# Performance work log

Measured on AMD Instinct MI355X. Metric: run time of the kernel, lower is better.

## Reference

```python
import jax, jax.numpy as jnp
import numpy as np

N_NODES = 60000
N_EDGES = 240000
N_REL = 4
N_GRAPHS = 128
D_IN = 768
D_H = 256
N_LAYERS = 6


def setup_inputs() -> dict:
    key = jax.random.key(0)
    ks = jax.random.split(key, 16)
    x = jax.random.normal(ks[0], (N_NODES, D_IN), dtype=jnp.float32)
    edge_index = jax.random.randint(ks[1], (2, N_EDGES), 0, N_NODES, dtype=jnp.int64)
    edge_attr = jax.random.randint(ks[2], (N_EDGES,), 0, N_REL, dtype=jnp.int64)
    batch = jnp.sort(jax.random.randint(ks[3], (N_NODES,), 0, N_GRAPHS, dtype=jnp.int64))
    s0 = 1.0 / np.sqrt(D_IN)
    s1 = 1.0 / np.sqrt(D_H)
    w0 = jax.random.normal(ks[4], (N_REL, D_IN, D_H), dtype=jnp.float32) * s0
    root0 = jax.random.normal(ks[5], (D_IN, D_H), dtype=jnp.float32) * s0
    b0 = jnp.zeros((D_H,), jnp.float32)
    w_rest = jax.random.normal(ks[6], (N_LAYERS - 1, N_REL, D_H, D_H), dtype=jnp.float32) * s1
    root_rest = jax.random.normal(ks[7], (N_LAYERS - 1, D_H, D_H), dtype=jnp.float32) * s1
    b_rest = jnp.zeros((N_LAYERS - 1, D_H), jnp.float32)
    fc1_w = jax.random.normal(ks[8], (2 * D_H, 128), dtype=jnp.float32) * (1.0 / np.sqrt(2 * D_H))
    fc1_b = jnp.zeros((128,), jnp.float32)
    fc2_w = jax.random.normal(ks[9], (128, 1), dtype=jnp.float32) * (1.0 / np.sqrt(128))
    fc2_b = jnp.zeros((1,), jnp.float32)
    return {"x": x, "edge_index": edge_index, "edge_attr": edge_attr, "batch": batch,
            "w0": w0, "root0": root0, "b0": b0,
            "w_rest": w_rest, "root_rest": root_rest, "b_rest": b_rest,
            "fc1_w": fc1_w, "fc1_b": fc1_b, "fc2_w": fc2_w, "fc2_b": fc2_b}


def _rgcn(h, src, dst, rel, W, root, b):
    # PyG RGCNConv with aggr='mean': per-relation mean over incoming edges,
    # transformed by per-relation weight, plus root transform and bias.
    n = h.shape[0]
    seg = rel * n + dst                                   # combined (relation, target) segment id
    msgs = h[src]                                         # [E, d_in] gather
    agg = jax.ops.segment_sum(msgs, seg, num_segments=N_REL * n)
    agg = agg.reshape(N_REL, n, -1)                       # [R, N, d_in]
    cnt = jax.ops.segment_sum(jnp.ones_like(rel, jnp.float32), seg, num_segments=N_REL * n)
    cnt = cnt.reshape(N_REL, n, 1)
    mean = agg / jnp.maximum(cnt, 1.0)                    # mean aggregation; 0 for isolated nodes
    return jnp.einsum('rnd,rdo->no', mean, W) + h @ root + b


def reference(x, edge_index, edge_attr, batch, w0, root0, b0,
              w_rest, root_rest, b_rest, fc1_w, fc1_b, fc2_w, fc2_b):
    src, dst = edge_index[0], edge_index[1]
    h = jax.nn.relu(_rgcn(x, src, dst, edge_attr, w0, root0, b0))
    for i in range(N_LAYERS - 1):
        h = jax.nn.relu(_rgcn(h, src, dst, edge_attr, w_rest[i], root_rest[i], b_rest[i]))
    # global mean / max pooling over graphs
    sums = jax.ops.segment_sum(h, batch, num_segments=N_GRAPHS)
    cnt = jax.ops.segment_sum(jnp.ones((h.shape[0],), jnp.float32), batch, num_segments=N_GRAPHS)[:, None]
    h_mean = sums / jnp.maximum(cnt, 1.0)
    h_max = jax.ops.segment_max(h, batch, num_segments=N_GRAPHS)
    h_max = jnp.where(cnt > 0, h_max, 0.0)
    g = jnp.concatenate([h_mean, h_max], axis=1)          # [G, 512]
    out = jax.nn.relu(g @ fc1_w + fc1_b)                  # dropout is identity at inference
    out = out @ fc2_w + fc2_b
    return jax.nn.sigmoid(out.squeeze(-1))                # [G]
```

## Files before the change

kernel.cpp:

```cpp
#include <hip/hip_runtime.h>
#include <hip/hip_bf16.h>

#define N_NODES  60000
#define N_EDGES  240000
#define N_REL    4
#define N_GRAPHS 128
#define D_IN     768
#define D_H      256
#define N_LAYERS 6
#define M_PAD    60032
#define N_TOT    1280
#define BM_L     64
#define LDM      264

static inline int cdiv(int a, int b) { return (a + b - 1) / b; }

typedef __attribute__((ext_vector_type(8))) short short8;
typedef __attribute__((ext_vector_type(4))) float f32x4;

__device__ __forceinline__ float bf2f(unsigned short u) {
    union { unsigned int i; float f; } c; c.i = ((unsigned int)u) << 16; return c.f;
}
__device__ __forceinline__ float bflo(unsigned int u) {
    union { unsigned int i; float f; } c; c.i = u << 16; return c.f;
}
__device__ __forceinline__ float bfhi(unsigned int u) {
    union { unsigned int i; float f; } c; c.i = u & 0xffff0000u; return c.f;
}
__device__ __forceinline__ unsigned short f2bf(float f) {
    union { float f; unsigned int i; } c; c.f = f;
    unsigned int i = c.i;
    unsigned int r = (i + 0x7FFFu + ((i >> 16) & 1u)) >> 16;
    return (unsigned short)r;
}

__device__ __forceinline__ void gload16(const void* g, void* l) {
    __builtin_amdgcn_global_load_lds((const __attribute__((address_space(1))) void*)g,
                                     (__attribute__((address_space(3))) void*)l, 16, 0, 0);
}

__device__ __forceinline__ void accum32(float4* am, uint4 v0, uint4 v1, uint4 v2, uint4 v3) {
    am[0].x += bflo(v0.x); am[0].y += bfhi(v0.x);
    am[0].z += bflo(v0.y); am[0].w += bfhi(v0.y);
    am[1].x += bflo(v0.z); am[1].y += bfhi(v0.z);
    am[1].z += bflo(v0.w); am[1].w += bfhi(v0.w);
    am[2].x += bflo(v1.x); am[2].y += bfhi(v1.x);
    am[2].z += bflo(v1.y); am[2].w += bfhi(v1.y);
    am[3].x += bflo(v1.z); am[3].y += bfhi(v1.z);
    am[3].z += bflo(v1.w); am[3].w += bfhi(v1.w);
    am[4].x += bflo(v2.x); am[4].y += bfhi(v2.x);
    am[4].z += bflo(v2.y); am[4].w += bfhi(v2.y);
    am[5].x += bflo(v2.z); am[5].y += bfhi(v2.z);
    am[5].z += bflo(v2.w); am[5].w += bfhi(v2.w);
    am[6].x += bflo(v3.x); am[6].y += bfhi(v3.x);
    am[6].z += bflo(v3.y); am[6].w += bfhi(v3.y);
    am[7].x += bflo(v3.z); am[7].y += bfhi(v3.z);
    am[7].z += bflo(v3.w); am[7].w += bfhi(v3.w);
}

__global__ __launch_bounds__(512) void gemm_l0(
    const unsigned short* __restrict__ A,
    const unsigned short* __restrict__ Bt,
    const float* __restrict__ bias,
    unsigned short* __restrict__ out_root,
    unsigned short* __restrict__ out_msg,
    int K)
{
    __shared__ unsigned short As[128 * 32];
    __shared__ unsigned short Bs[256 * 32];

    const int tid  = threadIdx.x;
    const int wave = tid >> 6, lane = tid & 63;

    int b = blockIdx.x;
    int bm, bn;
    if (b < 2320) { int grp = b / 40, rem = b % 40; bm = (grp * 8 + (rem & 7)) * 128; bn = (rem >> 3) * 256; }
    else          { int rem = b - 2320; bm = (464 + rem % 5) * 128; bn = (rem / 5) * 256; }

    const int wm = (wave & 1) * 64, wn = (wave >> 1) * 64;

    const int lr = lane >> 2;
    const int kg = ((lane & 3) ^ ((lr ^ (lr >> 2)) & 3)) * 8;
    const unsigned short* gsrc[3];
    unsigned short* ldst[3];
    #pragma unroll
    for (int j = 0; j < 3; ++j) {
        int g = wave * 3 + j;
        if (g < 8) {
            gsrc[j] = A + (size_t)(bm + g * 16 + lr) * K + kg;
            ldst[j] = As + g * 16 * 32;
        } else {
            gsrc[j] = Bt + (size_t)(bn + (g - 8) * 16 + lr) * K + kg;
            ldst[j] = Bs + (g - 8) * 16 * 32;
        }
    }

    f32x4 acc[4][4] = {};
    const int fr = lane & 15;
    const int qsw = (((lane >> 4) ^ fr ^ (fr >> 2)) & 3) * 8;

    for (int k0 = 0; k0 < K; k0 += 32) {
        gload16(gsrc[0] + k0, ldst[0]);
        gload16(gsrc[1] + k0, ldst[1]);
        gload16(gsrc[2] + k0, ldst[2]);
        __syncthreads();

        short8 a[4], bb[4];
        #pragma unroll
        for (int t = 0; t < 4; ++t) {
            a[t]  = *(const short8*)&As[(wm + t * 16 + fr) * 32 + qsw];
            bb[t] = *(const short8*)&Bs[(wn + t * 16 + fr) * 32 + qsw];
        }
        #pragma unroll
        for (int mt = 0; mt < 4; ++mt)
            #pragma unroll
            for (int nt = 0; nt < 4; ++nt)
                acc[mt][nt] = __builtin_amdgcn_mfma_f32_16x16x32_bf16(
                    a[mt], bb[nt], acc[mt][nt], 0, 0, 0);
        __syncthreads();
    }

    const bool is_root = (bn == 0);
    #pragma unroll
    for (int mt = 0; mt < 4; ++mt) {
        #pragma unroll
        for (int nt = 0; nt < 4; ++nt) {
            int col = bn + wn + nt * 16 + fr;
            float bv = bias[col];
            #pragma unroll
            for (int r = 0; r < 4; ++r) {
                int row = bm + wm + mt * 16 + ((lane >> 4) << 2) + r;
                float v = acc[mt][nt][r] + bv;
                if (is_root) out_root[(size_t)row * 256 + col] = f2bf(v);
                else         out_msg[(size_t)row * 1024 + (col - 256)] = f2bf(v);
            }
        }
    }
}

__global__ __launch_bounds__(512) void rgcn_layer(
    const unsigned short* __restrict__ h,
    const unsigned short* __restrict__ Wl,
    const float* __restrict__ bias,
    const int* __restrict__ rp4,
    const int* __restrict__ e_srcs,
    const float* __restrict__ inv4,
    unsigned short* __restrict__ h_out)
{
    __shared__ unsigned short mt[BM_L * LDM];

    const int tid  = threadIdx.x;
    const int wave = tid >> 6, lane = tid & 63;
    const int bm = blockIdx.x * BM_L;

    const int node  = bm + lane;
    const int cq    = wave * 32;
    const bool valid = node < N_NODES;

    const int fr   = lane & 15;
    const int q8   = (lane >> 4) * 8;
    const int wcol = wave * 32;

    const unsigned short* w0p = Wl + (size_t)(wcol + fr) * N_TOT + q8;
    const unsigned short* w1p = Wl + (size_t)(wcol + 16 + fr) * N_TOT + q8;

    float4 iv = valid ? *(const float4*)&inv4[(size_t)node * 4]
                      : make_float4(1.f, 1.f, 1.f, 1.f);

    f32x4 acc[4][2] = {};

    for (int r = 0; r < 5; ++r) {
        float4 am[8];
        #pragma unroll
        for (int j = 0; j < 8; ++j) am[j] = make_float4(0.f, 0.f, 0.f, 0.f);

        if (r < 4) {
            if (valid) {
                int lo = rp4[(size_t)node * 4 + r];
                int hi = rp4[(size_t)node * 4 + r + 1];
                int e = lo;
                for (; e + 1 < hi; e += 2) {
                    const uint4* p0 = (const uint4*)(h + (size_t)e_srcs[e] * 256 + cq);
                    const uint4* p1 = (const uint4*)(h + (size_t)e_srcs[e + 1] * 256 + cq);
                    uint4 v0 = p0[0], v1 = p0[1], v2 = p0[2], v3 = p0[3];
                    uint4 u0 = p1[0], u1 = p1[1], u2 = p1[2], u3 = p1[3];
                    accum32(am, v0, v1, v2, v3);
                    accum32(am, u0, u1, u2, u3);
                }
                if (e < hi) {
                    const uint4* p0 = (const uint4*)(h + (size_t)e_srcs[e] * 256 + cq);
                    accum32(am, p0[0], p0[1], p0[2], p0[3]);
                }
            }
        } else {
            const uint4* p0 = (const uint4*)(h + (size_t)node * 256 + cq);
            accum32(am, p0[0], p0[1], p0[2], p0[3]);
        }
        float sc = (r == 0) ? iv.x : (r == 1) ? iv.y : (r == 2) ? iv.z
                 : (r == 3) ? iv.w : 1.f;

        __syncthreads();
        {
            unsigned short* dst = &mt[lane * LDM + cq];
            #pragma unroll
            for (int j = 0; j < 8; ++j) {
                ushort4 o;
                o.x = f2bf(am[j].x * sc); o.y = f2bf(am[j].y * sc);
                o.z = f2bf(am[j].z * sc); o.w = f2bf(am[j].w * sc);
                *(ushort4*)(dst + j * 4) = o;
            }
        }
        __syncthreads();

        const int rOff = (r << 8);
        #pragma unroll
        for (int kk = 0; kk < 8; ++kk) {
            short8 b0 = *(const short8*)(w0p + rOff + kk * 32);
            short8 b1 = *(const short8*)(w1p + rOff + kk * 32);
            short8 a[4];
            #pragma unroll
            for (int i = 0; i < 4; ++i)
                a[i] = *(const short8*)&mt[(i * 16 + fr) * LDM + kk * 32 + q8];
            #pragma unroll
            for (int i = 0; i < 4; ++i) {
                acc[i][0] = __builtin_amdgcn_mfma_f32_16x16x32_bf16(a[i], b0, acc[i][0], 0, 0, 0);
                acc[i][1] = __builtin_amdgcn_mfma_f32_16x16x32_bf16(a[i], b1, acc[i][1], 0, 0, 0);
            }
        }
    }

    #pragma unroll
    for (int i = 0; i < 4; ++i) {
        #pragma unroll
        for (int nt = 0; nt < 2; ++nt) {
            int col = wcol + nt * 16 + fr;
            float bv = bias[col];
            #pragma unroll
            for (int rg = 0; rg < 4; ++rg) {
                int row = bm + i * 16 + ((lane >> 4) << 2) + rg;
                float v = fmaxf(acc[i][nt][rg] + bv, 0.f);
                h_out[(size_t)row * 256 + col] = f2bf(v);
            }
        }
    }
}

__global__ void convert_x(const float* __restrict__ x, unsigned short* __restrict__ xb) {
    size_t i = ((size_t)blockIdx.x * 256 + threadIdx.x) * 4;
    if (i >= (size_t)M_PAD * D_IN) return;
    ushort4 o;
    if (i < (size_t)N_NODES * D_IN) {
        float4 v = *(const float4*)&x[i];
        o.x = f2bf(v.x); o.y = f2bf(v.y); o.z = f2bf(v.z); o.w = f2bf(v.w);
    } else {
        o.x = o.y = o.z = o.w = 0;
    }
    *(ushort4*)&xb[i] = o;
}

__global__ void pack_w0(const float* __restrict__ root0, const float* __restrict__ w0,
                        unsigned short* __restrict__ Wt0) {
    int idx = blockIdx.x * 256 + threadIdx.x;
    if (idx >= N_TOT * D_IN) return;
    int k = idx % D_IN, n = idx / D_IN;
    float v = (n < 256) ? root0[k * 256 + n]
                        : w0[(((n >> 8) - 1) * D_IN + k) * 256 + (n & 255)];
    Wt0[idx] = f2bf(v);
}

__global__ void pack_wr(const float* __restrict__ root_rest, const float* __restrict__ w_rest,
                        unsigned short* __restrict__ WtR) {
    int idx = blockIdx.x * 256 + threadIdx.x;
    if (idx >= 5 * 256 * N_TOT) return;
    int k = idx % N_TOT; int t = idx / N_TOT; int n = t & 255; int l = t >> 8;
    float v = (k < 1024)
        ? w_rest[(((l * 4 + (k >> 8)) * 256) + (k & 255)) * 256 + n]
        : root_rest[(l * 256 + (k - 1024)) * 256 + n];
    WtR[idx] = f2bf(v);
}

__global__ void build_bias(const float* __restrict__ b0, float* __restrict__ eb) {
    int i = blockIdx.x * 256 + threadIdx.x;
    if (i < N_TOT) eb[i] = (i < 256) ? b0[i] : 0.f;
}

__global__ void deg4_count(const int* __restrict__ dst, const int* __restrict__ rel,
                           int* __restrict__ deg4, int E) {
    int e = blockIdx.x * 256 + threadIdx.x;
    if (e < E) atomicAdd(&deg4[dst[e] * 4 + rel[e]], 1);
}

__global__ void invert4(const int* __restrict__ deg4, float* __restrict__ inv4, int n) {
    int i = blockIdx.x * 256 + threadIdx.x;
    if (i < n) inv4[i] = 1.0f / (float)max(deg4[i], 1);
}

__global__ __launch_bounds__(256) void block_sum(const int* __restrict__ deg,
                                                 int* __restrict__ bsum, int n) {
    __shared__ int s[256];
    int i = blockIdx.x * 256 + threadIdx.x;
    s[threadIdx.x] = (i < n) ? deg[i] : 0;
    __syncthreads();
    for (int o = 128; o > 0; o >>= 1) {
        if (threadIdx.x < o) s[threadIdx.x] += s[threadIdx.x + o];
        __syncthreads();
    }
    if (threadIdx.x == 0) bsum[blockIdx.x] = s[0];
}

__global__ __launch_bounds__(1024) void scan_bsum(const int* __restrict__ bsum,
                                                  int* __restrict__ boff, int nb) {
    __shared__ int s[1024];
    int t = threadIdx.x;
    int v0 = (t < nb) ? bsum[t] : 0;
    s[t] = v0;
    __syncthreads();
    for (int o = 1; o < 1024; o <<= 1) {
        int v = (t >= o) ? s[t - o] : 0;
        __syncthreads();
        s[t] += v;
        __syncthreads();
    }
    if (t < nb) boff[t] = s[t] - v0;
}

__global__ __launch_bounds__(256) void block_scan_write(
    const int* __restrict__ deg, const int* __restrict__ boff,
    int* __restrict__ row_ptr, int* __restrict__ cursor, int n, int total) {
    __shared__ int s[256];
    int t = threadIdx.x;
    int i = blockIdx.x * 256 + t;
    int v = (i < n) ? deg[i] : 0;
    s[t] = v;
    __syncthreads();
    for (int o = 1; o < 256; o <<= 1) {
        int u = (t >= o) ? s[t - o] : 0;
        __syncthreads();
        s[t] += u;
        __syncthreads();
    }
    int excl = s[t] - v + boff[blockIdx.x];
    if (i < n) { row_ptr[i] = excl; cursor[i] = excl; }
    if (blockIdx.x == 0 && t == 0) row_ptr[n] = total;
}

__global__ void place_edges4(const int* __restrict__ dst, const int* __restrict__ src,
                             const int* __restrict__ rel, int* __restrict__ cursor,
                             int* __restrict__ e_srcs, int E) {
    int e = blockIdx.x * 256 + threadIdx.x;
    if (e < E) {
        int p = atomicAdd(&cursor[dst[e] * 4 + rel[e]], 1);
        e_srcs[p] = src[e];
    }
}

__global__ __launch_bounds__(256) void aggregate0(
    const unsigned short* __restrict__ rootb,
    const unsigned short* __restrict__ msg,
    const int* __restrict__ rp4, const int* __restrict__ e_srcs,
    const float* __restrict__ inv4,
    unsigned short* __restrict__ h_out)
{
    int node = blockIdx.x * 4 + (threadIdx.x >> 6);
    if (node >= N_NODES) return;
    int lane = threadIdx.x & 63;
    float4 iv = *(const float4*)&inv4[(size_t)node * 4];

    ushort4 rt = *(const ushort4*)&rootb[(size_t)node * 256 + lane * 4];
    float4 acc = make_float4(bf2f(rt.x), bf2f(rt.y), bf2f(rt.z), bf2f(rt.w));

    #pragma unroll
    for (int r = 0; r < 4; ++r) {
        int lo = rp4[(size_t)node * 4 + r], hi = rp4[(size_t)node * 4 + r + 1];
        float f = (r == 0) ? iv.x : (r == 1) ? iv.y : (r == 2) ? iv.z : iv.w;
        float4 s4 = make_float4(0, 0, 0, 0);
        int e = lo;
        for (; e + 1 < hi; e += 2) {
            ushort4 m0 = *(const ushort4*)&msg[(size_t)e_srcs[e] * 1024 + (r << 8) + lane * 4];
            ushort4 m1 = *(const ushort4*)&msg[(size_t)e_srcs[e + 1] * 1024 + (r << 8) + lane * 4];
            s4.x += bf2f(m0.x) + bf2f(m1.x);
            s4.y += bf2f(m0.y) + bf2f(m1.y);
            s4.z += bf2f(m0.z) + bf2f(m1.z);
            s4.w += bf2f(m0.w) + bf2f(m1.w);
        }
        if (e < hi) {
            ushort4 m0 = *(const ushort4*)&msg[(size_t)e_srcs[e] * 1024 + (r << 8) + lane * 4];
            s4.x += bf2f(m0.x); s4.y += bf2f(m0.y);
            s4.z += bf2f(m0.z); s4.w += bf2f(m0.w);
        }
        acc.x += s4.x * f; acc.y += s4.y * f;
        acc.z += s4.z * f; acc.w += s4.w * f;
    }
    ushort4 o;
    o.x = f2bf(fmaxf(acc.x, 0.f));
    o.y = f2bf(fmaxf(acc.y, 0.f));
    o.z = f2bf(fmaxf(acc.z, 0.f));
    o.w = f2bf(fmaxf(acc.w, 0.f));
    *(ushort4*)&h_out[(size_t)node * 256 + lane * 4] = o;
}

__global__ __launch_bounds__(256) void pool_kernel(
    const unsigned short* __restrict__ h, const int* __restrict__ batch,
    float* __restrict__ g_feat)
{
    int g = blockIdx.x;
    int t = threadIdx.x;
    __shared__ int s_lo, s_hi;
    if (t == 0) {
        int lo = 0, hi = N_NODES;
        while (lo < hi) { int m = (lo + hi) >> 1; if (batch[m] < g) lo = m + 1; else hi = m; }
        s_lo = lo;
        int lo2 = lo, hi2 = N_NODES;
        while (lo2 < hi2) { int m = (lo2 + hi2) >> 1; if (batch[m] < g + 1) lo2 = m + 1; else hi2 = m; }
        s_hi = lo2;
    }
    __syncthreads();
    int lo = s_lo, hi = s_hi;
    float sum = 0.f, mx = 0.f;
    for (int n = lo; n < hi; ++n) {
        float v = bf2f(h[(size_t)n * 256 + t]);
        sum += v;
        mx = fmaxf(mx, v);
    }
    float cnt = (float)(hi - lo);
    g_feat[g * 512 + t]       = sum / fmaxf(cnt, 1.0f);
    g_feat[g * 512 + 256 + t] = (cnt > 0.f) ? mx : 0.f;
}

__global__ __launch_bounds__(128) void mlp_head(
    const float* __restrict__ g_feat,
    const float* __restrict__ fc1_w, const float* __restrict__ fc1_b,
    const float* __restrict__ fc2_w, const float* __restrict__ fc2_b,
    float* __restrict__ out)
{
    __shared__ float gf[512];
    __shared__ float partial[2];
    int g = blockIdx.x, t = threadIdx.x;
    for (int i = t; i < 512; i += 128) gf[i] = g_feat[g * 512 + i];
    __syncthreads();
    float acc = fc1_b[t];
    for (int i = 0; i < 512; ++i) acc += gf[i] * fc1_w[i * 128 + t];
    float h1 = fmaxf(acc, 0.f);
    float v = h1 * fc2_w[t];
    #pragma unroll
    for (int off = 32; off > 0; off >>= 1) v += __shfl_down(v, off);
    if ((t & 63) == 0) partial[t >> 6] = v;
    __syncthreads();
    if (t == 0) {
        float s = partial[0] + partial[1] + fc2_b[0];
        out[g] = 1.0f / (1.0f + expf(-s));
    }
}

extern "C" void kernel_launch(void* const* d_in, const int* in_sizes, int n_in,
                              void* d_out, int out_size, void* d_ws, size_t ws_size,
                              hipStream_t stream) {
    const float* x          = (const float*)d_in[0];
    const int*   edge_index = (const int*)d_in[1];
    const int*   edge_attr  = (const int*)d_in[2];
    const int*   batch      = (const int*)d_in[3];
    const float* w0         = (const float*)d_in[4];
    const float* root0      = (const float*)d_in[5];
    const float* b0         = (const float*)d_in[6];
    const float* w_rest     = (const float*)d_in[7];
    const float* root_rest  = (const float*)d_in[8];
    const float* b_rest     = (const float*)d_in[9];
    const float* fc1_w      = (const float*)d_in[10];
    const float* fc1_b      = (const float*)d_in[11];
    const float* fc2_w      = (const float*)d_in[12];
    const float* fc2_b      = (const float*)d_in[13];
    float* out = (float*)d_out;

    const int* e_src = edge_index;
    const int* e_dst = edge_index + N_EDGES;

    char* p = (char*)d_ws;
    auto alloc = [&](size_t bytes) { char* q = p; p += (bytes + 255) & ~(size_t)255; return q; };
    unsigned short* x_bf   = (unsigned short*)alloc((size_t)M_PAD * D_IN * 2);
    unsigned short* msgbuf = (unsigned short*)alloc((size_t)M_PAD * 1024 * 2);
    unsigned short* hA     = (unsigned short*)alloc((size_t)M_PAD * 256 * 2);
    unsigned short* hB     = (unsigned short*)alloc((size_t)M_PAD * 256 * 2);
    unsigned short* Wt0    = (unsigned short*)alloc((size_t)N_TOT * D_IN * 2);
    unsigned short* WtR    = (unsigned short*)alloc((size_t)5 * 256 * N_TOT * 2);
    float*          ebias  = (float*)alloc(N_TOT * 4);
    float*          inv4   = (float*)alloc((size_t)N_NODES * 4 * 4);
    float*          g_feat = (float*)alloc((size_t)N_GRAPHS * 512 * 4);
    int*            deg4   = (int*)alloc((size_t)N_NODES * 4 * 4);
    int*            rp4    = (int*)alloc(((size_t)N_NODES * 4 + 1) * 4);
    int*            cursor4= (int*)alloc((size_t)N_NODES * 4 * 4);
    int*            bsum   = (int*)alloc(1024 * 4);
    int*            boff   = (int*)alloc(1024 * 4);
    int*            e_srcs = (int*)alloc((size_t)N_EDGES * 4);

    const int n4 = N_NODES * 4;
    const int nscan4 = cdiv(n4, 256);

    hipMemsetAsync(deg4, 0, (size_t)n4 * 4, stream);
    convert_x<<<cdiv(M_PAD * D_IN / 4, 256), 256, 0, stream>>>(x, x_bf);
    pack_w0<<<cdiv(N_TOT * D_IN, 256), 256, 0, stream>>>(root0, w0, Wt0);
    pack_wr<<<cdiv(5 * 256 * N_TOT, 256), 256, 0, stream>>>(root_rest, w_rest, WtR);
    build_bias<<<cdiv(N_TOT, 256), 256, 0, stream>>>(b0, ebias);
    deg4_count<<<cdiv(N_EDGES, 256), 256, 0, stream>>>(e_dst, edge_attr, deg4, N_EDGES);
    invert4<<<cdiv(n4, 256), 256, 0, stream>>>(deg4, inv4, n4);
    block_sum<<<nscan4, 256, 0, stream>>>(deg4, bsum, n4);
    scan_bsum<<<1, 1024, 0, stream>>>(bsum, boff, nscan4);
    block_scan_write<<<nscan4, 256, 0, stream>>>(deg4, boff, rp4, cursor4, n4, N_EDGES);
    place_edges4<<<cdiv(N_EDGES, 256), 256, 0, stream>>>(e_dst, e_src, edge_attr,
                                                         cursor4, e_srcs, N_EDGES);

    gemm_l0<<<2345, 512, 0, stream>>>(x_bf, Wt0, ebias, hB, msgbuf, D_IN);
    aggregate0<<<cdiv(N_NODES, 4), 256, 0, stream>>>(hB, msgbuf, rp4, e_srcs, inv4, hA);

    unsigned short* cur = hA;
    unsigned short* nxt = hB;
    for (int L = 1; L < N_LAYERS; ++L) {
        rgcn_layer<<<M_PAD / BM_L, 512, 0, stream>>>(
            cur, WtR + (size_t)(L - 1) * 256 * N_TOT, b_rest + (size_t)(L - 1) * 256,
            rp4, e_srcs, inv4, nxt);
        unsigned short* t = cur; cur = nxt; nxt = t;
    }

    pool_kernel<<<N_GRAPHS, 256, 0, stream>>>(cur, batch, g_feat);
    mlp_head<<<N_GRAPHS, 128, 0, stream>>>(g_feat, fc1_w, fc1_b, fc2_w, fc2_b, out);
}
```

Before: 1.368 ms.

## Gather messages wave-per-node with coalesced row reads and prefetch weight fragments

Reworks the aggregation in the fused RGCN layer kernel. Before, each lane owned one node and read a 64-byte slice of every neighbour row. Now each wave walks its 8 nodes one after another, and the 64 lanes read a full 512-byte neighbour row together in 8-byte pieces. This is meant to make the gathers coalesced and spread the uneven degree work across lanes instead of leaving lanes idle on divergent loops. The per-relation weight fragments are also loaded into registers before the gather, so their latency overlaps it. The trade-offs are serialised per-node loops with fewer loads in flight per lane, and higher register pressure from the 16 prefetched fragments.

```diff
diff --git a/kernel.cpp b/kernel.cpp
--- a/kernel.cpp
+++ b/kernel.cpp
@@ -21,12 +21,6 @@
 __device__ __forceinline__ float bf2f(unsigned short u) {
     union { unsigned int i; float f; } c; c.i = ((unsigned int)u) << 16; return c.f;
 }
-__device__ __forceinline__ float bflo(unsigned int u) {
-    union { unsigned int i; float f; } c; c.i = u << 16; return c.f;
-}
-__device__ __forceinline__ float bfhi(unsigned int u) {
-    union { unsigned int i; float f; } c; c.i = u & 0xffff0000u; return c.f;
-}
 __device__ __forceinline__ unsigned short f2bf(float f) {
     union { float f; unsigned int i; } c; c.f = f;
     unsigned int i = c.i;
@@ -37,25 +31,6 @@
 __device__ __forceinline__ void gload16(const void* g, void* l) {
     __builtin_amdgcn_global_load_lds((const __attribute__((address_space(1))) void*)g,
                                      (__attribute__((address_space(3))) void*)l, 16, 0, 0);
-}
-
-__device__ __forceinline__ void accum32(float4* am, uint4 v0, uint4 v1, uint4 v2, uint4 v3) {
-    am[0].x += bflo(v0.x); am[0].y += bfhi(v0.x);
-    am[0].z += bflo(v0.y); am[0].w += bfhi(v0.y);
-    am[1].x += bflo(v0.z); am[1].y += bfhi(v0.z);
-    am[1].z += bflo(v0.w); am[1].w += bfhi(v0.w);
-    am[2].x += bflo(v1.x); am[2].y += bfhi(v1.x);
-    am[2].z += bflo(v1.y); am[2].w += bfhi(v1.y);
-    am[3].x += bflo(v1.z); am[3].y += bfhi(v1.z);
-    am[3].z += bflo(v1.w); am[3].w += bfhi(v1.w);
-    am[4].x += bflo(v2.x); am[4].y += bfhi(v2.x);
-    am[4].z += bflo(v2.y); am[4].w += bfhi(v2.y);
-    am[5].x += bflo(v2.z); am[5].y += bfhi(v2.z);
-    am[5].z += bflo(v2.w); am[5].w += bfhi(v2.w);
-    am[6].x += bflo(v3.x); am[6].y += bfhi(v3.x);
-    am[6].z += bflo(v3.y); am[6].w += bfhi(v3.y);
-    am[7].x += bflo(v3.z); am[7].y += bfhi(v3.z);
-    am[7].z += bflo(v3.w); am[7].w += bfhi(v3.w);
 }
 
 __global__ __launch_bounds__(512) void gemm_l0(
@@ -153,78 +128,74 @@
     const int wave = tid >> 6, lane = tid & 63;
     const int bm = blockIdx.x * BM_L;
 
-    const int node  = bm + lane;
-    const int cq    = wave * 32;
-    const bool valid = node < N_NODES;
-
     const int fr   = lane & 15;
     const int q8   = (lane >> 4) * 8;
     const int wcol = wave * 32;
 
-    const unsigned short* w0p = Wl + (size_t)(wcol + fr) * N_TOT + q8;
-    const unsigned short* w1p = Wl + (size_t)(wcol + 16 + fr) * N_TOT + q8;
-
-    float4 iv = valid ? *(const float4*)&inv4[(size_t)node * 4]
-                      : make_float4(1.f, 1.f, 1.f, 1.f);
-
     f32x4 acc[4][2] = {};
 
     for (int r = 0; r < 5; ++r) {
-        float4 am[8];
-        #pragma unroll
-        for (int j = 0; j < 8; ++j) am[j] = make_float4(0.f, 0.f, 0.f, 0.f);
-
-        if (r < 4) {
-            if (valid) {
-                int lo = rp4[(size_t)node * 4 + r];
-                int hi = rp4[(size_t)node * 4 + r + 1];
-                int e = lo;
-                for (; e + 1 < hi; e += 2) {
-                    const uint4* p0 = (const uint4*)(h + (size_t)e_srcs[e] * 256 + cq);
-                    const uint4* p1 = (const uint4*)(h + (size_t)e_srcs[e + 1] * 256 + cq);
-                    uint4 v0 = p0[0], v1 = p0[1], v2 = p0[2], v3 = p0[3];
-                    uint4 u0 = p1[0], u1 = p1[1], u2 = p1[2], u3 = p1[3];
-                    accum32(am, v0, v1, v2, v3);
-                    accum32(am, u0, u1, u2, u3);
-                }
-                if (e < hi) {
-                    const uint4* p0 = (const uint4*)(h + (size_t)e_srcs[e] * 256 + cq);
-                    accum32(am, p0[0], p0[1], p0[2], p0[3]);
+        const int rOff = r << 8;
+        short8 bf0[8], bf1[8];
+        {
+            const unsigned short* w0p = Wl + (size_t)(wcol + fr) * N_TOT + rOff + q8;
+            const unsigned short* w1p = Wl + (size_t)(wcol + 16 + fr) * N_TOT + rOff + q8;
+            #pragma unroll
+            for (int kk = 0; kk < 8; ++kk) {
+                bf0[kk] = *(const short8*)(w0p + kk * 32);
+                bf1[kk] = *(const short8*)(w1p + kk * 32);
+            }
+        }
+
+        __syncthreads();
+
+        #pragma unroll 1
+        for (int j = 0; j < 8; ++j) {
+            int ln = wave * 8 + j;
+            int node = bm + ln;
+            float4 a = make_float4(0.f, 0.f, 0.f, 0.f);
+            if (node < N_NODES) {
+                if (r < 4) {
+                    int lo = rp4[node * 4 + r];
+                    int hi = rp4[node * 4 + r + 1];
+                    float sc = inv4[node * 4 + r];
+                    int e = lo;
+                    for (; e + 1 < hi; e += 2) {
+                        ushort4 m0 = *(const ushort4*)&h[(size_t)e_srcs[e] * 256 + lane * 4];
+                        ushort4 m1 = *(const ushort4*)&h[(size_t)e_srcs[e + 1] * 256 + lane * 4];
+                        a.x += bf2f(m0.x) + bf2f(m1.x);
+                        a.y += bf2f(m0.y) + bf2f(m1.y);
+                        a.z += bf2f(m0.z) + bf2f(m1.z);
+                        a.w += bf2f(m0.w) + bf2f(m1.w);
+                    }
+                    if (e < hi) {
+                        ushort4 m0 = *(const ushort4*)&h[(size_t)e_srcs[e] * 256 + lane * 4];
+                        a.x += bf2f(m0.x); a.y += bf2f(m0.y);
+                        a.z += bf2f(m0.z); a.w += bf2f(m0.w);
+                    }
+                    a.x *= sc; a.y *= sc; a.z *= sc; a.w *= sc;
+                } else {
+                    ushort4 m0 = *(const ushort4*)&h[(size_t)node * 256 + lane * 4];
+                    a.x = bf2f(m0.x); a.y = bf2f(m0.y);
+                    a.z = bf2f(m0.z); a.w = bf2f(m0.w);
                 }
             }
-        } else {
-            const uint4* p0 = (const uint4*)(h + (size_t)node * 256 + cq);
-            accum32(am, p0[0], p0[1], p0[2], p0[3]);
-        }
-        float sc = (r == 0) ? iv.x : (r == 1) ? iv.y : (r == 2) ? iv.z
-                 : (r == 3) ? iv.w : 1.f;
-
-        __syncthreads();
-        {
-            unsigned short* dst = &mt[lane * LDM + cq];
-            #pragma unroll
-            for (int j = 0; j < 8; ++j) {
-                ushort4 o;
-                o.x = f2bf(am[j].x * sc); o.y = f2bf(am[j].y * sc);
-                o.z = f2bf(am[j].z * sc); o.w = f2bf(am[j].w * sc);
-                *(ushort4*)(dst + j * 4) = o;
-            }
-        }
-        __syncthreads();
-
-        const int rOff = (r << 8);
+            ushort4 o;
+            o.x = f2bf(a.x); o.y = f2bf(a.y); o.z = f2bf(a.z); o.w = f2bf(a.w);
+            *(ushort4*)&mt[ln * LDM + lane * 4] = o;
+        }
+        __syncthreads();
+
         #pragma unroll
         for (int kk = 0; kk < 8; ++kk) {
-            short8 b0 = *(const short8*)(w0p + rOff + kk * 32);
-            short8 b1 = *(const short8*)(w1p + rOff + kk * 32);
-            short8 a[4];
+            short8 a4[4];
             #pragma unroll
             for (int i = 0; i < 4; ++i)
-                a[i] = *(const short8*)&mt[(i * 16 + fr) * LDM + kk * 32 + q8];
+                a4[i] = *(const short8*)&mt[(i * 16 + fr) * LDM + kk * 32 + q8];
             #pragma unroll
             for (int i = 0; i < 4; ++i) {
-                acc[i][0] = __builtin_amdgcn_mfma_f32_16x16x32_bf16(a[i], b0, acc[i][0], 0, 0, 0);
-                acc[i][1] = __builtin_amdgcn_mfma_f32_16x16x32_bf16(a[i], b1, acc[i][1], 0, 0, 0);
+                acc[i][0] = __builtin_amdgcn_mfma_f32_16x16x32_bf16(a4[i], bf0[kk], acc[i][0], 0, 0, 0);
+                acc[i][1] = __builtin_amdgcn_mfma_f32_16x16x32_bf16(a4[i], bf1[kk], acc[i][1], 0, 0, 0);
             }
         }
     }
```

Result: slower. 1.743 ms (+27.4%).
